# Kernel tuning notes

Hardware: AMD Instinct MI355X
Metric: run time of the kernel (lower is better)

Reference implementation:

```python
import jax, jax.numpy as jnp
import numpy as np

B = 128
DIM = 1024


def setup_inputs() -> dict:
    key = jax.random.key(0)
    k1, k2 = jax.random.split(key)
    return {
        "input1": jax.random.normal(k1, (B, DIM), dtype=jnp.float32),
        "input2": jax.random.normal(k2, (B, DIM), dtype=jnp.float32),
    }


def reference(input1, input2):
    # Original torch module computes, via a dim x dim x dim permutation tensor:
    #   cc[b, i] = sum_t input1[b, (i - t) % dim] * input2[b, t]   (circular convolution)
    # then sums over the batch and reshapes to [1, 1, dim].
    dim = input1.shape[1]
    # idx[i, t] = (i - t) mod dim  -> circulant gather of input1
    idx = (jnp.arange(dim)[:, None] - jnp.arange(dim)[None, :]) % dim
    gathered = input1[:, idx]                      # [B, dim, dim]
    cc = jnp.einsum('bit,bt->bi', gathered, input2)  # per-batch circular conv [B, dim]
    sum_rep = jnp.sum(cc, axis=0)                  # [dim]
    return sum_rep[None, None, :]                  # [1, 1, dim]
```

## Files before the change

### kernel.cpp

```cpp
#include <hip/hip_runtime.h>


#define CC_D 1024

__device__ __forceinline__ float bcast(float v, int lane) {
  return __int_as_float(__builtin_amdgcn_readlane(__float_as_int(v), lane));
}

__global__ __launch_bounds__(256, 8) void cc_partial_kernel(
    const float* __restrict__ X, const float* __restrict__ Y,
    float* __restrict__ ws) {
  const int blk    = blockIdx.x;
  const int b      = blk >> 4;
  const int tslice = blk & 15;
  const int tid    = threadIdx.x;
  const int lane   = tid & 63;

  __shared__ __align__(16) float4 sm4[512];

  const int t0 = tslice * 64;

  const float4 xv   = ((const float4*)(X + b * CC_D))[tid];
  const float ymine = Y[b * CC_D + t0 + lane];
  sm4[tid]       = xv;
  sm4[tid + 256] = xv;
  __syncthreads();

  const int fbase = tid + 254 - 16 * tslice;

  float W[12];
  {
    const float4 w0 = sm4[fbase];
    const float4 w1 = sm4[fbase + 1];
    const float4 w2 = sm4[fbase + 2];
    W[0] = w0.x; W[1]  = w0.y; W[2]  = w0.z; W[3]  = w0.w;
    W[4] = w1.x; W[5]  = w1.y; W[6]  = w1.z; W[7]  = w1.w;
    W[8] = w2.x; W[9]  = w2.y; W[10] = w2.z; W[11] = w2.w;
  }

  float4 acc = make_float4(0.f, 0.f, 0.f, 0.f);

#pragma unroll
  for (int g = 0; g < 8; ++g) {
#pragma unroll
    for (int r = 0; r < 8; ++r) {
      const float ybc = bcast(ymine, 8 * g + r);
      acc.x += W[8 - r]  * ybc;
      acc.y += W[9 - r]  * ybc;
      acc.z += W[10 - r] * ybc;
      acc.w += W[11 - r] * ybc;
    }
    if (g < 7) {
      W[8] = W[0]; W[9] = W[1]; W[10] = W[2]; W[11] = W[3];
      const float4 w0 = sm4[fbase - 2 * (g + 1)];
      const float4 w1 = sm4[fbase - 2 * (g + 1) + 1];
      W[0] = w0.x; W[1] = w0.y; W[2] = w0.z; W[3] = w0.w;
      W[4] = w1.x; W[5] = w1.y; W[6] = w1.z; W[7] = w1.w;
    }
  }

  ((float4*)ws)[(size_t)tid * 2048 + blk] = acc;
}

__global__ __launch_bounds__(256) void cc_reduce_kernel(
    const float* __restrict__ ws, float* __restrict__ out) {
  const int j   = blockIdx.x;
  const int tid = threadIdx.x;
  const int l   = tid & 63;
  const int w   = tid >> 6;

  __shared__ float4 red[4];

  const float4* row = (const float4*)ws + (size_t)j * 2048;
  float4 s = make_float4(0.f, 0.f, 0.f, 0.f);
#pragma unroll
  for (int c = 0; c < 8; ++c) {
    const float4 v = row[(size_t)(c * 256 + tid)];
    s.x += v.x; s.y += v.y; s.z += v.z; s.w += v.w;
  }
#pragma unroll
  for (int o = 32; o > 0; o >>= 1) {
    s.x += __shfl_xor(s.x, o, 64);
    s.y += __shfl_xor(s.y, o, 64);
    s.z += __shfl_xor(s.z, o, 64);
    s.w += __shfl_xor(s.w, o, 64);
  }
  if (l == 0) red[w] = s;
  __syncthreads();

  if (tid == 0) {
    float4 r = red[0];
    r.x += red[1].x + red[2].x + red[3].x;
    r.y += red[1].y + red[2].y + red[3].y;
    r.z += red[1].z + red[2].z + red[3].z;
    r.w += red[1].w + red[2].w + red[3].w;
    ((float4*)out)[j] = r;
  }
}

extern "C" void kernel_launch(void* const* d_in, const int* in_sizes, int n_in,
                              void* d_out, int out_size, void* d_ws,
                              size_t ws_size, hipStream_t stream) {
  const float* X = (const float*)d_in[0];
  const float* Y = (const float*)d_in[1];
  float* out = (float*)d_out;
  float* ws  = (float*)d_ws;

  cc_partial_kernel<<<2048, 256, 0, stream>>>(X, Y, ws);
  cc_reduce_kernel<<<256, 256, 0, stream>>>(ws, out);
}
```

Baseline: 70.05 us.

## Widen partial blocks to 1024 threads and pre-reduce partials in shared memory

Each partial block now handles half of one batch row's t-range, using four 256-thread groups that each cover 128 t values over 16 groups of 8 broadcasts, instead of 16 blocks of 64 t values. The four group accumulators are summed in shared memory before a single store, which shrinks the workspace written and read by the reduce kernel by a factor of eight. The cost is only 256 blocks, fewer than the CU count on this GPU, plus extra barriers and longer serial work per thread.

```diff
diff --git a/kernel.cpp b/kernel.cpp
--- a/kernel.cpp
+++ b/kernel.cpp
@@ -7,32 +7,34 @@
   return __int_as_float(__builtin_amdgcn_readlane(__float_as_int(v), lane));
 }
 
-__global__ __launch_bounds__(256, 8) void cc_partial_kernel(
+__global__ __launch_bounds__(1024, 4) void cc_partial_kernel(
     const float* __restrict__ X, const float* __restrict__ Y,
     float* __restrict__ ws) {
-  const int blk    = blockIdx.x;
-  const int b      = blk >> 4;
-  const int tslice = blk & 15;
-  const int tid    = threadIdx.x;
-  const int lane   = tid & 63;
+  const int blk   = blockIdx.x;
+  const int b     = blk >> 1;
+  const int thalf = blk & 1;
+  const int tid   = threadIdx.x;
+  const int ig    = tid & 255;
+  const int q     = tid >> 8;
+  const int lane  = tid & 63;
 
-  __shared__ __align__(16) float4 sm4[512];
+  __shared__ __align__(16) float smem[4096];
+  float4* sm4 = (float4*)smem;
 
-  const int t0 = tslice * 64;
+  const int t0 = thalf * 512 + q * 128;
 
-  const float4 xv   = ((const float4*)(X + b * CC_D))[tid];
-  const float ymine = Y[b * CC_D + t0 + lane];
-  sm4[tid]       = xv;
-  sm4[tid + 256] = xv;
+  if (tid < 512) sm4[tid] = ((const float4*)(X + b * CC_D))[tid & 255];
+  const float y0 = Y[b * CC_D + t0 + lane];
+  const float y1 = Y[b * CC_D + t0 + 64 + lane];
   __syncthreads();
 
-  const int fbase = tid + 254 - 16 * tslice;
+  const int fb0 = 254 + ig - (t0 >> 2);
 
   float W[12];
   {
-    const float4 w0 = sm4[fbase];
-    const float4 w1 = sm4[fbase + 1];
-    const float4 w2 = sm4[fbase + 2];
+    const float4 w0 = sm4[fb0];
+    const float4 w1 = sm4[fb0 + 1];
+    const float4 w2 = sm4[fb0 + 2];
     W[0] = w0.x; W[1]  = w0.y; W[2]  = w0.z; W[3]  = w0.w;
     W[4] = w1.x; W[5]  = w1.y; W[6]  = w1.z; W[7]  = w1.w;
     W[8] = w2.x; W[9]  = w2.y; W[10] = w2.z; W[11] = w2.w;
@@ -41,25 +43,41 @@
   float4 acc = make_float4(0.f, 0.f, 0.f, 0.f);
 
 #pragma unroll
-  for (int g = 0; g < 8; ++g) {
+  for (int g = 0; g < 16; ++g) {
+    const float ysrc = (g < 8) ? y0 : y1;
 #pragma unroll
     for (int r = 0; r < 8; ++r) {
-      const float ybc = bcast(ymine, 8 * g + r);
+      const float ybc = bcast(ysrc, 8 * (g & 7) + r);
       acc.x += W[8 - r]  * ybc;
       acc.y += W[9 - r]  * ybc;
       acc.z += W[10 - r] * ybc;
       acc.w += W[11 - r] * ybc;
     }
-    if (g < 7) {
+    if (g < 15) {
       W[8] = W[0]; W[9] = W[1]; W[10] = W[2]; W[11] = W[3];
-      const float4 w0 = sm4[fbase - 2 * (g + 1)];
-      const float4 w1 = sm4[fbase - 2 * (g + 1) + 1];
+      const float4 w0 = sm4[fb0 - 2 * (g + 1)];
+      const float4 w1 = sm4[fb0 - 2 * (g + 1) + 1];
       W[0] = w0.x; W[1] = w0.y; W[2] = w0.z; W[3] = w0.w;
       W[4] = w1.x; W[5] = w1.y; W[6] = w1.z; W[7] = w1.w;
     }
   }
 
-  ((float4*)ws)[(size_t)tid * 2048 + blk] = acc;
+  __syncthreads();
+  ((float4*)smem)[q * 256 + ig] = acc;
+  __syncthreads();
+
+  if (tid < 256) {
+    const float4 s0 = ((const float4*)smem)[tid];
+    const float4 s1 = ((const float4*)smem)[256 + tid];
+    const float4 s2 = ((const float4*)smem)[512 + tid];
+    const float4 s3 = ((const float4*)smem)[768 + tid];
+    float4 s;
+    s.x = (s0.x + s1.x) + (s2.x + s3.x);
+    s.y = (s0.y + s1.y) + (s2.y + s3.y);
+    s.z = (s0.z + s1.z) + (s2.z + s3.z);
+    s.w = (s0.w + s1.w) + (s2.w + s3.w);
+    ((float4*)ws)[(size_t)tid * 256 + blk] = s;
+  }
 }
 
 __global__ __launch_bounds__(256) void cc_reduce_kernel(
@@ -71,13 +89,7 @@
 
   __shared__ float4 red[4];
 
-  const float4* row = (const float4*)ws + (size_t)j * 2048;
-  float4 s = make_float4(0.f, 0.f, 0.f, 0.f);
-#pragma unroll
-  for (int c = 0; c < 8; ++c) {
-    const float4 v = row[(size_t)(c * 256 + tid)];
-    s.x += v.x; s.y += v.y; s.z += v.z; s.w += v.w;
-  }
+  float4 s = ((const float4*)ws)[(size_t)j * 256 + tid];
 #pragma unroll
   for (int o = 32; o > 0; o >>= 1) {
     s.x += __shfl_xor(s.x, o, 64);
@@ -106,6 +118,6 @@
   float* out = (float*)d_out;
   float* ws  = (float*)d_ws;
 
-  cc_partial_kernel<<<2048, 256, 0, stream>>>(X, Y, ws);
+  cc_partial_kernel<<<256, 1024, 0, stream>>>(X, Y, ws);
   cc_reduce_kernel<<<256, 256, 0, stream>>>(ws, out);
 }
```

Measured after the change: 66.91 us. 4.5% less time.
